# Performance work log

Measured on AMD Instinct MI355X. Metric: run time of the kernel, lower is better.

## Reference

```python
import jax, jax.numpy as jnp
import numpy as np

S, D, E = 16384, 4096, 64
CAPACITY_FACTOR = 1.25  # training mode
CAPACITY = int(CAPACITY_FACTOR * S / E)  # 320


def setup_inputs() -> dict:
    key = jax.random.key(0)
    kx, kw = jax.random.split(key)
    x = jax.random.normal(kx, (S, D), dtype=jnp.float32)
    W_g = jax.random.normal(kw, (E, D), dtype=jnp.float32) * (1.0 / np.sqrt(D))
    return {"x": x, "W_g": W_g}


def reference(x, W_g):
    # Router GEMM + softmax.  x: [S, D], W_g: [E, D] (nn.Linear weight layout).
    S_ = x.shape[0]
    E_ = W_g.shape[0]
    logits = x @ W_g.T                       # [S, E]
    gates = jax.nn.softmax(logits, axis=-1)  # [S, E]

    # Top-2 experts per token (topk is constant across the original per-token loop,
    # so we compute it once).
    vals, idx = jax.lax.top_k(gates, 2)
    g1, g2 = vals[:, 0], vals[:, 1]          # [S]
    e1, e2 = idx[:, 0], idx[:, 1]            # [S] int32
    denom = g1 + g2
    g1n = g1 / denom                         # normalized top-1 gate
    g2n = g2 / denom                         # normalized top-2 gate

    # Pass 1: top-1 dispatch, capacity-limited, serialized in token order.
    # cumsum of one-hot gives each token its 1-indexed position within its expert.
    m1 = jax.nn.one_hot(e1, E_, dtype=gates.dtype)              # [S, E]
    pos1 = jnp.sum(jnp.cumsum(m1, axis=0) * m1, axis=-1)        # [S]
    keep1 = pos1 <= CAPACITY                                    # [S] bool
    counts1 = jnp.sum(m1 * keep1[:, None].astype(gates.dtype), axis=0)  # [E]

    # Pass 2: top-2 dispatch with random keep prob (rnd < 2*g2n), capacity-limited
    # against the counts remaining after pass 1, again serialized in token order.
    rnd = jax.random.uniform(jax.random.key(1), (S_,), dtype=gates.dtype)
    want2 = rnd < 2.0 * g2n                                     # [S] bool
    m2 = jax.nn.one_hot(e2, E_, dtype=gates.dtype) * want2[:, None].astype(gates.dtype)
    pos2 = jnp.sum(jnp.cumsum(m2, axis=0) * m2, axis=-1)        # [S]
    keep2 = want2 & (pos2 <= (CAPACITY - counts1)[e2])          # [S] bool

    rows = jnp.arange(S_)
    combine = jnp.zeros_like(gates)
    combine = combine.at[rows, e1].set(jnp.where(keep1, g1n, 0.0))
    combine = combine.at[rows, e2].set(jnp.where(keep2, g2n, 0.0))
    return combine
```

## Files before the change

kernel.cpp:

```cpp
#include <hip/hip_runtime.h>
#include <stdint.h>

#define S 16384
#define D 4096
#define NE 64
#define CAP 320
#define WQ 8
#define KCH (D / WQ)
#define KSTEPS (KCH / 16)
#define NKS (D / 16)
#define K2ROWS 128
#define NB (S / K2ROWS)

typedef _Float16 f16x8 __attribute__((ext_vector_type(8)));
typedef float f32x16 __attribute__((ext_vector_type(16)));

__device__ __forceinline__ uint32_t rotl32(uint32_t v, int n) {
  return (v << n) | (v >> (32 - n));
}

__device__ uint32_t threefry_bits(int i) {
  const uint32_t k0 = 0u, k1 = 1u;
  const uint32_t ks2 = k0 ^ k1 ^ 0x1BD11BDAu;
  uint32_t x0 = 0u + k0;
  uint32_t x1 = (uint32_t)i + k1;
#define TFR(R) { x0 += x1; x1 = rotl32(x1, R); x1 ^= x0; }
  TFR(13) TFR(15) TFR(26) TFR(6)
  x0 += k1;  x1 += ks2 + 1u;
  TFR(17) TFR(29) TFR(16) TFR(24)
  x0 += ks2; x1 += k0 + 2u;
  TFR(13) TFR(15) TFR(26) TFR(6)
  x0 += k0;  x1 += k1 + 3u;
  TFR(17) TFR(29) TFR(16) TFR(24)
  x0 += k1;  x1 += ks2 + 4u;
  TFR(13) TFR(15) TFR(26) TFR(6)
  x0 += ks2; x1 += k0 + 5u;
#undef TFR
  return x0 ^ x1;
}

__global__ __launch_bounds__(256) void k0_packw(const float* __restrict__ Wg,
                                                f16x8* __restrict__ WH,
                                                f16x8* __restrict__ WL) {
  const int tid = blockIdx.x * 256 + threadIdx.x;
  const int lane = tid & 63;
  const int t = (tid >> 6) & 1;
  const int ks = tid >> 7;
  const int col = 32 * t + (lane & 31);
  const int k0 = ks * 16 + 8 * (lane >> 5);
  const float* wp = Wg + (size_t)col * D + k0;
  f16x8 h, l;
#pragma unroll
  for (int j = 0; j < 8; ++j) {
    const float w = wp[j];
    const _Float16 wh = (_Float16)w;
    const float r = (w - (float)wh) * 4096.0f;
    h[j] = wh;
    l[j] = (_Float16)r;
  }
  WH[tid] = h;
  WL[tid] = l;
}

__global__ __launch_bounds__(512, 4) void k1_fused(const float* __restrict__ x,
                                                   const f16x8* __restrict__ WH,
                                                   const f16x8* __restrict__ WL,
                                                   int* __restrict__ E1, int* __restrict__ E2,
                                                   int* __restrict__ WANT,
                                                   float* __restrict__ G1, float* __restrict__ G2) {
  __shared__ float lsum[WQ][32][64];
  const int w = threadIdx.x >> 6;
  const int lane = threadIdx.x & 63;
  const int rowBase = blockIdx.x * 32;
  const int row = rowBase + (lane & 31);
  const float* xp = x + (size_t)row * D + w * KCH + (lane >> 5) * 8;
  const int ks0 = w * KSTEPS;

  f32x16 acc0[2], acc1[2];
#pragma unroll
  for (int t = 0; t < 2; ++t)
#pragma unroll
    for (int r = 0; r < 16; ++r) { acc0[t][r] = 0.0f; acc1[t][r] = 0.0f; }

  float4 a0 = *(const float4*)(xp);
  float4 a1 = *(const float4*)(xp + 4);
#pragma unroll 2
  for (int s = 0; s < KSTEPS; ++s) {
    const int sn = (s + 1 < KSTEPS) ? s + 1 : s;
    const float4 a0n = *(const float4*)(xp + sn * 16);
    const float4 a1n = *(const float4*)(xp + sn * 16 + 4);
    const size_t fi = (size_t)(ks0 + s) * 128 + lane;
    const f16x8 bh0 = WH[fi];
    const f16x8 bh1 = WH[fi + 64];
    const f16x8 bl0 = WL[fi];
    const f16x8 bl1 = WL[fi + 64];

    const float af[8] = {a0.x, a0.y, a0.z, a0.w, a1.x, a1.y, a1.z, a1.w};
    f16x8 ah, al;
#pragma unroll
    for (int j = 0; j < 8; ++j) {
      const _Float16 h = (_Float16)af[j];
      ah[j] = h;
      al[j] = (_Float16)((af[j] - (float)h) * 4096.0f);
    }

    acc0[0] = __builtin_amdgcn_mfma_f32_32x32x16_f16(ah, bh0, acc0[0], 0, 0, 0);
    acc1[0] = __builtin_amdgcn_mfma_f32_32x32x16_f16(al, bh0, acc1[0], 0, 0, 0);
    acc1[0] = __builtin_amdgcn_mfma_f32_32x32x16_f16(ah, bl0, acc1[0], 0, 0, 0);
    acc0[1] = __builtin_amdgcn_mfma_f32_32x32x16_f16(ah, bh1, acc0[1], 0, 0, 0);
    acc1[1] = __builtin_amdgcn_mfma_f32_32x32x16_f16(al, bh1, acc1[1], 0, 0, 0);
    acc1[1] = __builtin_amdgcn_mfma_f32_32x32x16_f16(ah, bl1, acc1[1], 0, 0, 0);

    a0 = a0n; a1 = a1n;
  }

#pragma unroll
  for (int t = 0; t < 2; ++t) {
    const int col = 32 * t + (lane & 31);
#pragma unroll
    for (int r = 0; r < 16; ++r) {
      const int lrow = (r & 3) + 8 * (r >> 2) + 4 * (lane >> 5);
      lsum[w][lrow][col] = acc0[t][r] + acc1[t][r] * (1.0f / 4096.0f);
    }
  }
  __syncthreads();

  {
    float* p0 = &lsum[0][0][0];
#pragma unroll
    for (int j = 0; j < 4; ++j) {
      const int idx = threadIdx.x + 512 * j;
      float v = p0[idx];
#pragma unroll
      for (int q = 1; q < WQ; ++q) v += (&lsum[0][0][0])[q * 2048 + idx];
      p0[idx] = v;
    }
  }
  __syncthreads();

  for (int rr = 0; rr < 4; ++rr) {
    const int lrow = w * 4 + rr;
    const int grow = rowBase + lrow;
    const float l = lsum[0][lrow][lane];

    float m = l;
#pragma unroll
    for (int off = 32; off; off >>= 1) m = fmaxf(m, __shfl_xor(m, off));
    const float ex = expf(l - m);
    float ssum = ex;
#pragma unroll
    for (int off = 32; off; off >>= 1) ssum += __shfl_xor(ssum, off);
    ssum = __shfl(ssum, 0);
    const float gate = ex / ssum;

    float v = gate; int id = lane;
#pragma unroll
    for (int off = 32; off; off >>= 1) {
      float vo = __shfl_xor(v, off); int io = __shfl_xor(id, off);
      if (vo > v || (vo == v && io < id)) { v = vo; id = io; }
    }
    const float g1 = v; const int e1 = id;
    const float gate2 = (lane == e1) ? -1.0f : gate;
    v = gate2; id = lane;
#pragma unroll
    for (int off = 32; off; off >>= 1) {
      float vo = __shfl_xor(v, off); int io = __shfl_xor(id, off);
      if (vo > v || (vo == v && io < id)) { v = vo; id = io; }
    }
    const float g2 = v; const int e2 = id;

    if (lane == 0) {
      const float denom = g1 + g2;
      const float g1n = g1 / denom;
      const float g2n = g2 / denom;
      const uint32_t bits = threefry_bits(grow);
      const float rnd = __uint_as_float((bits >> 9) | 0x3f800000u) - 1.0f;
      E1[grow] = e1; E2[grow] = e2;
      WANT[grow] = (rnd < 2.0f * g2n) ? 1 : 0;
      G1[grow] = g1n; G2[grow] = g2n;
    }
  }
}

__global__ __launch_bounds__(K2ROWS) void k2_rank(const int* __restrict__ E1,
                                                  const int* __restrict__ E2,
                                                  const int* __restrict__ WANT,
                                                  int* __restrict__ LR1, int* __restrict__ LR2,
                                                  int* __restrict__ H1, int* __restrict__ H2) {
  __shared__ unsigned char s1[K2ROWS], s2[K2ROWS];
  __shared__ int h1[NE], h2[NE];
  const int b = blockIdx.x, t = threadIdx.x;
  const int r = b * K2ROWS + t;
  if (t < NE) { h1[t] = 0; h2[t] = 0; }
  const int e1 = E1[r];
  const int e2 = WANT[r] ? E2[r] : NE;
  s1[t] = (unsigned char)e1;
  s2[t] = (unsigned char)e2;
  __syncthreads();
  int r1 = 0, r2 = 0;
  for (int j = 0; j < t; ++j) {
    r1 += (s1[j] == e1);
    r2 += (s2[j] == e2);
  }
  LR1[r] = r1; LR2[r] = r2;
  atomicAdd(&h1[e1], 1);
  if (e2 < NE) atomicAdd(&h2[e2], 1);
  __syncthreads();
  if (t < NE) { H1[b * NE + t] = h1[t]; H2[b * NE + t] = h2[t]; }
}

__global__ __launch_bounds__(256) void k3_prefix(const int* __restrict__ H1,
                                                 const int* __restrict__ H2,
                                                 int* __restrict__ OFF1, int* __restrict__ OFF2,
                                                 int* __restrict__ REM2) {
  __shared__ int sh1[NB * NE], sh2[NB * NE];
  const int t = threadIdx.x;
#pragma unroll
  for (int j = 0; j < 8; ++j) {
    const int i4 = t + 256 * j;
    ((int4*)sh1)[i4] = ((const int4*)H1)[i4];
    ((int4*)sh2)[i4] = ((const int4*)H2)[i4];
  }
  __syncthreads();
  if (t < NE) {
    int run1 = 0, run2 = 0;
    for (int b = 0; b < NB; ++b) {
      OFF1[b * NE + t] = run1; run1 += sh1[b * NE + t];
      OFF2[b * NE + t] = run2; run2 += sh2[b * NE + t];
    }
    REM2[t] = CAP - min(run1, CAP);
  }
}

__global__ __launch_bounds__(256) void k4_write(const int* __restrict__ E1,
                                                const int* __restrict__ E2,
                                                const int* __restrict__ WANT,
                                                const float* __restrict__ G1,
                                                const float* __restrict__ G2,
                                                const int* __restrict__ LR1,
                                                const int* __restrict__ LR2,
                                                const int* __restrict__ OFF1,
                                                const int* __restrict__ OFF2,
                                                const int* __restrict__ REM2,
                                                float* __restrict__ out) {
  const int w = threadIdx.x >> 6, lane = threadIdx.x & 63;
  const int rowBase = blockIdx.x * 16 + w * 4;
#pragma unroll
  for (int i = 0; i < 4; ++i) {
    const int r = rowBase + i;
    const int b = r / K2ROWS;
    const int e1 = E1[r];
    const int pos1 = OFF1[b * NE + e1] + LR1[r] + 1;
    float val = 0.0f;
    if (lane == e1 && pos1 <= CAP) val = G1[r];
    if (WANT[r]) {
      const int e2 = E2[r];
      const int pos2 = OFF2[b * NE + e2] + LR2[r] + 1;
      if (lane == e2 && pos2 <= REM2[e2]) val = G2[r];
    }
    out[(size_t)r * NE + lane] = val;
  }
}

extern "C" void kernel_launch(void* const* d_in, const int* in_sizes, int n_in,
                              void* d_out, int out_size, void* d_ws, size_t ws_size,
                              hipStream_t stream) {
  const float* x  = (const float*)d_in[0];
  const float* Wg = (const float*)d_in[1];
  float* out = (float*)d_out;
  char* ws = (char*)d_ws;

  size_t off = 0;
  int*   E1   = (int*)(ws + off);   off += (size_t)S * 4;
  int*   E2   = (int*)(ws + off);   off += (size_t)S * 4;
  int*   WANT = (int*)(ws + off);   off += (size_t)S * 4;
  float* G1   = (float*)(ws + off); off += (size_t)S * 4;
  float* G2   = (float*)(ws + off); off += (size_t)S * 4;
  int*   LR1  = (int*)(ws + off);   off += (size_t)S * 4;
  int*   LR2  = (int*)(ws + off);   off += (size_t)S * 4;
  int*   H1   = (int*)(ws + off);   off += (size_t)NB * NE * 4;
  int*   H2   = (int*)(ws + off);   off += (size_t)NB * NE * 4;
  int*   OFF1 = (int*)(ws + off);   off += (size_t)NB * NE * 4;
  int*   OFF2 = (int*)(ws + off);   off += (size_t)NB * NE * 4;
  int*   REM2 = (int*)(ws + off);   off += (size_t)NE * 4;
  f16x8* WH   = (f16x8*)(ws + off); off += (size_t)NKS * 2 * 64 * sizeof(f16x8);
  f16x8* WL   = (f16x8*)(ws + off); off += (size_t)NKS * 2 * 64 * sizeof(f16x8);

  k0_packw<<<128, 256, 0, stream>>>(Wg, WH, WL);
  k1_fused<<<S / 32, 512, 0, stream>>>(x, WH, WL, E1, E2, WANT, G1, G2);
  k2_rank<<<NB, K2ROWS, 0, stream>>>(E1, E2, WANT, LR1, LR2, H1, H2);
  k3_prefix<<<1, 256, 0, stream>>>(H1, H2, OFF1, OFF2, REM2);
  k4_write<<<S / 16, 256, 0, stream>>>(E1, E2, WANT, G1, G2, LR1, LR2, OFF1, OFF2, REM2, out);
}
```

Baseline: 395.8 us.

## Split router GEMM K across two blocks with separate softmax/top-2 reduce kernel

The fused GEMM+softmax kernel is split in two. A 256-thread logits kernel has each block cover half of the K range for 32 rows and write partial logits to a workspace buffer. A new reduce kernel sums the two partials and does the softmax, top-2 selection and random-keep decision. The GEMM loop is also manually double-buffered across two k-steps. The aim is more, smaller blocks for better occupancy and latency hiding, at the cost of an extra kernel launch and a 8 MB partial-logits round trip through memory.

Result: no change. 394.4 us (-0.3%).

```diff
diff --git a/kernel.cpp b/kernel.cpp
--- a/kernel.cpp
+++ b/kernel.cpp
@@ -5,8 +5,9 @@
 #define D 4096
 #define NE 64
 #define CAP 320
-#define WQ 8
-#define KCH (D / WQ)
+#define WPB 4
+#define KSPLIT 8
+#define KCH (D / KSPLIT)
 #define KSTEPS (KCH / 16)
 #define NKS (D / 16)
 #define K2ROWS 128
@@ -62,123 +63,131 @@
   WL[tid] = l;
 }
 
-__global__ __launch_bounds__(512, 4) void k1_fused(const float* __restrict__ x,
-                                                   const f16x8* __restrict__ WH,
-                                                   const f16x8* __restrict__ WL,
-                                                   int* __restrict__ E1, int* __restrict__ E2,
-                                                   int* __restrict__ WANT,
-                                                   float* __restrict__ G1, float* __restrict__ G2) {
-  __shared__ float lsum[WQ][32][64];
+#define CVT1(J, F)                                                     \
+  { const float f_ = (F); const _Float16 h_ = (_Float16)f_;            \
+    ah[J] = h_; al[J] = (_Float16)((f_ - (float)h_) * 4096.0f); }
+
+#define KSTEP(X0, X1, BH0, BH1, BL0, BL1)                                    \
+  {                                                                          \
+    f16x8 ah, al;                                                            \
+    CVT1(0, (X0).x) CVT1(1, (X0).y) CVT1(2, (X0).z) CVT1(3, (X0).w)          \
+    CVT1(4, (X1).x) CVT1(5, (X1).y) CVT1(6, (X1).z) CVT1(7, (X1).w)          \
+    acc00 = __builtin_amdgcn_mfma_f32_32x32x16_f16(ah, BH0, acc00, 0, 0, 0); \
+    acc10 = __builtin_amdgcn_mfma_f32_32x32x16_f16(al, BH0, acc10, 0, 0, 0); \
+    acc10 = __builtin_amdgcn_mfma_f32_32x32x16_f16(ah, BL0, acc10, 0, 0, 0); \
+    acc01 = __builtin_amdgcn_mfma_f32_32x32x16_f16(ah, BH1, acc01, 0, 0, 0); \
+    acc11 = __builtin_amdgcn_mfma_f32_32x32x16_f16(al, BH1, acc11, 0, 0, 0); \
+    acc11 = __builtin_amdgcn_mfma_f32_32x32x16_f16(ah, BL1, acc11, 0, 0, 0); \
+  }
+
+__global__ __launch_bounds__(256) void k1_logits(const float* __restrict__ x,
+                                                 const f16x8* __restrict__ WH,
+                                                 const f16x8* __restrict__ WL,
+                                                 float* __restrict__ part) {
+  __shared__ float lsum[WPB][32][64];
   const int w = threadIdx.x >> 6;
   const int lane = threadIdx.x & 63;
-  const int rowBase = blockIdx.x * 32;
+  const int rg = blockIdx.x >> 1;
+  const int kh = blockIdx.x & 1;
+  const int rowBase = rg * 32;
   const int row = rowBase + (lane & 31);
-  const float* xp = x + (size_t)row * D + w * KCH + (lane >> 5) * 8;
-  const int ks0 = w * KSTEPS;
-
-  f32x16 acc0[2], acc1[2];
-#pragma unroll
-  for (int t = 0; t < 2; ++t)
-#pragma unroll
-    for (int r = 0; r < 16; ++r) { acc0[t][r] = 0.0f; acc1[t][r] = 0.0f; }
-
-  float4 a0 = *(const float4*)(xp);
-  float4 a1 = *(const float4*)(xp + 4);
-#pragma unroll 2
-  for (int s = 0; s < KSTEPS; ++s) {
-    const int sn = (s + 1 < KSTEPS) ? s + 1 : s;
-    const float4 a0n = *(const float4*)(xp + sn * 16);
-    const float4 a1n = *(const float4*)(xp + sn * 16 + 4);
-    const size_t fi = (size_t)(ks0 + s) * 128 + lane;
-    const f16x8 bh0 = WH[fi];
-    const f16x8 bh1 = WH[fi + 64];
-    const f16x8 bl0 = WL[fi];
-    const f16x8 bl1 = WL[fi + 64];
-
-    const float af[8] = {a0.x, a0.y, a0.z, a0.w, a1.x, a1.y, a1.z, a1.w};
-    f16x8 ah, al;
+  const int kidx = kh * 4 + w;
+  const float* xp = x + (size_t)row * D + kidx * KCH + (lane >> 5) * 8;
+  const float4* xq = (const float4*)xp;
+  const int ks0 = kidx * KSTEPS;
+
+  f32x16 acc00, acc01, acc10, acc11;
+#pragma unroll
+  for (int r = 0; r < 16; ++r) { acc00[r] = 0.0f; acc01[r] = 0.0f; acc10[r] = 0.0f; acc11[r] = 0.0f; }
+
+  float4 xa0 = xq[0], xa1 = xq[1];
+  size_t fiA = (size_t)ks0 * 128 + lane;
+  f16x8 bha0 = WH[fiA], bha1 = WH[fiA + 64];
+  f16x8 bla0 = WL[fiA], bla1 = WL[fiA + 64];
+
+  for (int s = 0; s < KSTEPS; s += 2) {
+    const size_t fiB = (size_t)(ks0 + s + 1) * 128 + lane;
+    const float4 xb0 = xq[(s + 1) * 4];
+    const float4 xb1 = xq[(s + 1) * 4 + 1];
+    const f16x8 bhb0 = WH[fiB], bhb1 = WH[fiB + 64];
+    const f16x8 blb0 = WL[fiB], blb1 = WL[fiB + 64];
+
+    KSTEP(xa0, xa1, bha0, bha1, bla0, bla1);
+
+    const int s2 = (s + 2 < KSTEPS) ? (s + 2) : 0;
+    const size_t fiA2 = (size_t)(ks0 + s2) * 128 + lane;
+    xa0 = xq[s2 * 4]; xa1 = xq[s2 * 4 + 1];
+    bha0 = WH[fiA2]; bha1 = WH[fiA2 + 64];
+    bla0 = WL[fiA2]; bla1 = WL[fiA2 + 64];
+
+    KSTEP(xb0, xb1, bhb0, bhb1, blb0, blb1);
+  }
+
+#pragma unroll
+  for (int r = 0; r < 16; ++r) {
+    const int lrow = (r & 3) + 8 * (r >> 2) + 4 * (lane >> 5);
+    lsum[w][lrow][lane & 31]        = acc00[r] + acc10[r] * (1.0f / 4096.0f);
+    lsum[w][lrow][32 + (lane & 31)] = acc01[r] + acc11[r] * (1.0f / 4096.0f);
+  }
+  __syncthreads();
+
+  {
+    const float* p0 = &lsum[0][0][0];
 #pragma unroll
     for (int j = 0; j < 8; ++j) {
-      const _Float16 h = (_Float16)af[j];
-      ah[j] = h;
-      al[j] = (_Float16)((af[j] - (float)h) * 4096.0f);
+      const int idx = threadIdx.x + 256 * j;
+      const float v = ((p0[idx] + p0[idx + 2048]) + p0[idx + 4096]) + p0[idx + 6144];
+      part[((size_t)kh * S + rowBase) * NE + idx] = v;
     }
-
-    acc0[0] = __builtin_amdgcn_mfma_f32_32x32x16_f16(ah, bh0, acc0[0], 0, 0, 0);
-    acc1[0] = __builtin_amdgcn_mfma_f32_32x32x16_f16(al, bh0, acc1[0], 0, 0, 0);
-    acc1[0] = __builtin_amdgcn_mfma_f32_32x32x16_f16(ah, bl0, acc1[0], 0, 0, 0);
-    acc0[1] = __builtin_amdgcn_mfma_f32_32x32x16_f16(ah, bh1, acc0[1], 0, 0, 0);
-    acc1[1] = __builtin_amdgcn_mfma_f32_32x32x16_f16(al, bh1, acc1[1], 0, 0, 0);
-    acc1[1] = __builtin_amdgcn_mfma_f32_32x32x16_f16(ah, bl1, acc1[1], 0, 0, 0);
-
-    a0 = a0n; a1 = a1n;
-  }
-
-#pragma unroll
-  for (int t = 0; t < 2; ++t) {
-    const int col = 32 * t + (lane & 31);
-#pragma unroll
-    for (int r = 0; r < 16; ++r) {
-      const int lrow = (r & 3) + 8 * (r >> 2) + 4 * (lane >> 5);
-      lsum[w][lrow][col] = acc0[t][r] + acc1[t][r] * (1.0f / 4096.0f);
-    }
-  }
-  __syncthreads();
-
-  {
-    float* p0 = &lsum[0][0][0];
-#pragma unroll
-    for (int j = 0; j < 4; ++j) {
-      const int idx = threadIdx.x + 512 * j;
-      float v = p0[idx];
-#pragma unroll
-      for (int q = 1; q < WQ; ++q) v += (&lsum[0][0][0])[q * 2048 + idx];
-      p0[idx] = v;
-    }
-  }
-  __syncthreads();
-
-  for (int rr = 0; rr < 4; ++rr) {
-    const int lrow = w * 4 + rr;
-    const int grow = rowBase + lrow;
-    const float l = lsum[0][lrow][lane];
-
-    float m = l;
-#pragma unroll
-    for (int off = 32; off; off >>= 1) m = fmaxf(m, __shfl_xor(m, off));
-    const float ex = expf(l - m);
-    float ssum = ex;
-#pragma unroll
-    for (int off = 32; off; off >>= 1) ssum += __shfl_xor(ssum, off);
-    ssum = __shfl(ssum, 0);
-    const float gate = ex / ssum;
-
-    float v = gate; int id = lane;
-#pragma unroll
-    for (int off = 32; off; off >>= 1) {
-      float vo = __shfl_xor(v, off); int io = __shfl_xor(id, off);
-      if (vo > v || (vo == v && io < id)) { v = vo; id = io; }
-    }
-    const float g1 = v; const int e1 = id;
-    const float gate2 = (lane == e1) ? -1.0f : gate;
-    v = gate2; id = lane;
-#pragma unroll
-    for (int off = 32; off; off >>= 1) {
-      float vo = __shfl_xor(v, off); int io = __shfl_xor(id, off);
-      if (vo > v || (vo == v && io < id)) { v = vo; id = io; }
-    }
-    const float g2 = v; const int e2 = id;
-
-    if (lane == 0) {
-      const float denom = g1 + g2;
-      const float g1n = g1 / denom;
-      const float g2n = g2 / denom;
-      const uint32_t bits = threefry_bits(grow);
-      const float rnd = __uint_as_float((bits >> 9) | 0x3f800000u) - 1.0f;
-      E1[grow] = e1; E2[grow] = e2;
-      WANT[grow] = (rnd < 2.0f * g2n) ? 1 : 0;
-      G1[grow] = g1n; G2[grow] = g2n;
-    }
+  }
+}
+
+__global__ __launch_bounds__(256) void k1b_reduce(const float* __restrict__ part,
+                                                  int* __restrict__ E1, int* __restrict__ E2,
+                                                  int* __restrict__ WANT,
+                                                  float* __restrict__ G1, float* __restrict__ G2) {
+  const int row = blockIdx.x * 4 + (threadIdx.x >> 6);
+  const int lane = threadIdx.x & 63;
+  float l = 0.0f;
+#pragma unroll
+  for (int c = 0; c < 2; ++c)
+    l += part[((size_t)c * S + row) * NE + lane];
+
+  float m = l;
+#pragma unroll
+  for (int off = 32; off; off >>= 1) m = fmaxf(m, __shfl_xor(m, off));
+  const float ex = expf(l - m);
+  float ssum = ex;
+#pragma unroll
+  for (int off = 32; off; off >>= 1) ssum += __shfl_xor(ssum, off);
+  ssum = __shfl(ssum, 0);
+  const float gate = ex / ssum;
+
+  float v = gate; int id = lane;
+#pragma unroll
+  for (int off = 32; off; off >>= 1) {
+    float vo = __shfl_xor(v, off); int io = __shfl_xor(id, off);
+    if (vo > v || (vo == v && io < id)) { v = vo; id = io; }
+  }
+  const float g1 = v; const int e1 = id;
+  const float gate2 = (lane == e1) ? -1.0f : gate;
+  v = gate2; id = lane;
+#pragma unroll
+  for (int off = 32; off; off >>= 1) {
+    float vo = __shfl_xor(v, off); int io = __shfl_xor(id, off);
+    if (vo > v || (vo == v && io < id)) { v = vo; id = io; }
+  }
+  const float g2 = v; const int e2 = id;
+
+  if (lane == 0) {
+    const float denom = g1 + g2;
+    const float g1n = g1 / denom;
+    const float g2n = g2 / denom;
+    const uint32_t bits = threefry_bits(row);
+    const float rnd = __uint_as_float((bits >> 9) | 0x3f800000u) - 1.0f;
+    E1[row] = e1; E2[row] = e2;
+    WANT[row] = (rnd < 2.0f * g2n) ? 1 : 0;
+    G1[row] = g1n; G2[row] = g2n;
   }
 }
 
@@ -271,6 +280,7 @@
   char* ws = (char*)d_ws;
 
   size_t off = 0;
+  float* part = (float*)ws;         off += (size_t)2 * S * NE * 4;
   int*   E1   = (int*)(ws + off);   off += (size_t)S * 4;
   int*   E2   = (int*)(ws + off);   off += (size_t)S * 4;
   int*   WANT = (int*)(ws + off);   off += (size_t)S * 4;
@@ -287,7 +297,8 @@
   f16x8* WL   = (f16x8*)(ws + off); off += (size_t)NKS * 2 * 64 * sizeof(f16x8);
 
   k0_packw<<<128, 256, 0, stream>>>(Wg, WH, WL);
-  k1_fused<<<S / 32, 512, 0, stream>>>(x, WH, WL, E1, E2, WANT, G1, G2);
+  k1_logits<<<(S / 32) * 2, 256, 0, stream>>>(x, WH, WL, part);
+  k1b_reduce<<<S / 4, 256, 0, stream>>>(part, E1, E2, WANT, G1, G2);
   k2_rank<<<NB, K2ROWS, 0, stream>>>(E1, E2, WANT, LR1, LR2, H1, H2);
   k3_prefix<<<1, 256, 0, stream>>>(H1, H2, OFF1, OFF2, REM2);
   k4_write<<<S / 16, 256, 0, stream>>>(E1, E2, WANT, G1, G2, LR1, LR2, OFF1, OFF2, REM2, out);
```
